# Kernel optimization log

Hardware: AMD Instinct MI355X
Metric: run time of the kernel (lower is better)

The kernel has to match this reference:

```python
import jax, jax.numpy as jnp
import numpy as np

TEMP = 0.07  # softmax temperature T


def _l2norm(x, axis=1, eps=1e-12):
    return x / jnp.clip(jnp.linalg.norm(x, axis=axis, keepdims=True), eps, None)


def setup_inputs() -> dict:
    key = jax.random.key(0)
    k1, k2, k3, k4 = jax.random.split(key, 4)
    B, K, D = 256, 8192, 128
    q = jax.random.normal(k1, (B, D), dtype=jnp.float32)
    ba_queue = _l2norm(jax.random.normal(k2, (K, D), dtype=jnp.float32))
    nonba_queue = _l2norm(jax.random.normal(k3, (K, D), dtype=jnp.float32))
    targets = jax.random.randint(k4, (B,), 0, 2, dtype=jnp.int64)
    return {"q": q, "ba_queue": ba_queue, "nonba_queue": nonba_queue, "targets": targets}


def reference(q, ba_queue, nonba_queue, targets):
    K = ba_queue.shape[0]
    # encoder output is L2-normalized; queues are detached buffers
    qn = _l2norm(q, axis=1)
    all_feature = jnp.concatenate([qn, ba_queue, nonba_queue], axis=0)  # [N, D]
    all_label = jnp.concatenate([
        targets.astype(jnp.int32),
        jnp.ones((K,), dtype=jnp.int32),
        jnp.zeros((K,), dtype=jnp.int32),
    ])  # [N]
    N = all_feature.shape[0]

    # [N, N] similarity logits
    sim = jnp.matmul(all_feature, all_feature.T) / TEMP
    logits = sim - jax.lax.stop_gradient(jnp.max(sim, axis=1, keepdims=True))

    # positive mask (same label), excluding self
    mask = (all_label[:, None] == all_label[None, :]).astype(jnp.float32)
    logits_mask = 1.0 - jnp.eye(N, dtype=jnp.float32)
    mask = mask * logits_mask

    exp_logits = jnp.exp(logits) * logits_mask
    log_prob = logits - jnp.log(jnp.sum(exp_logits, axis=1, keepdims=True))
    mean_log_prob_pos = jnp.sum(mask * log_prob, axis=1) / jnp.sum(mask, axis=1)
    return -jnp.mean(mean_log_prob_pos)
```

## Files before the change

### kernel.cpp

```cpp
#include <hip/hip_runtime.h>
#include <hip/hip_bf16.h>
#include <stdint.h>

#define TEMPERATURE 0.07f
#define SC 20.6099312f

constexpr int NQ = 256;
constexpr int KQ = 8192;
constexpr int D  = 128;
constexpr int N  = NQ + 2 * KQ;
constexpr int CS = 26;
constexpr int BN = 128;
constexpr int NT = N / BN;
constexpr int RBM = N / 128;
constexpr int RBF = N / 256;

typedef float f32x16 __attribute__((ext_vector_type(16)));
typedef int   i32x4  __attribute__((ext_vector_type(4)));
typedef int   i32x8  __attribute__((ext_vector_type(8)));

constexpr size_t OFF_F32  = 0;
constexpr size_t OFF_8    = OFF_F32  + (size_t)N * D * 4;
constexpr size_t OFF_8S   = OFF_8    + (size_t)N * D;
constexpr size_t OFF_PART = OFF_8S   + (size_t)N * D;
constexpr size_t OFF_LP   = OFF_PART + (size_t)CS * N * 4;
constexpr size_t OFF_S    = OFF_LP   + (size_t)260 * 2 * 128 * 4;
constexpr size_t OFF_CNT  = OFF_S    + 2 * 128 * 4;
constexpr size_t OFF_BSUM = OFF_CNT  + 16;

__global__ __launch_bounds__(256) void k_prep(const float* __restrict__ q,
                                              const float* __restrict__ ba,
                                              const float* __restrict__ nb,
                                              const long long* __restrict__ tgt,
                                              float* __restrict__ ff,
                                              unsigned char* __restrict__ fb8,
                                              unsigned char* __restrict__ fb8s,
                                              float* __restrict__ lp) {
    __shared__ float red[4][2][128];
    int wid = threadIdx.x >> 6, lane = threadIdx.x & 63;
    int rbase = blockIdx.x * 64 + wid * 16;
    float s0x = 0.f, s0y = 0.f, s1x = 0.f, s1y = 0.f;
    for (int i = 0; i < 16; ++i) {
        int r = rbase + i;
        const float* src = (r < NQ) ? (q + (size_t)r * D)
                         : (r < NQ + KQ) ? (ba + (size_t)(r - NQ) * D)
                         : (nb + (size_t)(r - NQ - KQ) * D);
        float2 v = *(const float2*)(src + lane * 2);
        float a = v.x, b = v.y;
        int lab;
        if (r < NQ) {
            float ss = a * a + b * b;
            #pragma unroll
            for (int m = 1; m < 64; m <<= 1) ss += __shfl_xor(ss, m);
            float scale = 1.0f / fmaxf(sqrtf(ss), 1e-12f);
            a *= scale; b *= scale;
            lab = (int)tgt[r];
        } else {
            lab = (r < NQ + KQ) ? 1 : 0;
        }
        *(float2*)(ff + (size_t)r * D + lane * 2) = make_float2(a, b);
        int w8  = __builtin_amdgcn_cvt_pk_fp8_f32(a, b, 0, false);
        int w8s = __builtin_amdgcn_cvt_pk_fp8_f32(a * SC, b * SC, 0, false);
        *(unsigned short*)(fb8  + (size_t)r * D + lane * 2) = (unsigned short)w8;
        *(unsigned short*)(fb8s + (size_t)r * D + lane * 2) = (unsigned short)w8s;
        if (lab) { s1x += a; s1y += b; } else { s0x += a; s0y += b; }
    }
    red[wid][0][lane * 2]     = s0x;
    red[wid][0][lane * 2 + 1] = s0y;
    red[wid][1][lane * 2]     = s1x;
    red[wid][1][lane * 2 + 1] = s1y;
    __syncthreads();
    int lab2 = threadIdx.x >> 7, d = threadIdx.x & 127;
    float s = red[0][lab2][d] + red[1][lab2][d] + red[2][lab2][d] + red[3][lab2][d];
    lp[((size_t)blockIdx.x * 2 + lab2) * 128 + d] = s;
}

__global__ __launch_bounds__(256) void k_lsum_b(const float* __restrict__ lp,
                                                const long long* __restrict__ tgt,
                                                float* __restrict__ S,
                                                int* __restrict__ cnt) {
    int lab = threadIdx.x >> 7;
    int d   = threadIdx.x & 127;
    float s[4] = {0.f, 0.f, 0.f, 0.f};
    for (int b = 0; b < 260; b += 4) {
        #pragma unroll
        for (int j = 0; j < 4; ++j)
            s[j] += lp[((size_t)(b + j) * 2 + lab) * 128 + d];
    }
    S[lab * 128 + d] = (s[0] + s[1]) + (s[2] + s[3]);
    if (threadIdx.x < 64) {
        int c = 0;
        #pragma unroll
        for (int i = 0; i < 4; ++i) c += (int)tgt[threadIdx.x + 64 * i];
        #pragma unroll
        for (int m = 1; m < 64; m <<= 1) c += __shfl_xor(c, m);
        if (threadIdx.x == 0) { cnt[0] = (NQ - c) + KQ; cnt[1] = c + KQ; }
    }
}

__global__ __launch_bounds__(256, 4) void k_main(const unsigned char* __restrict__ fb8,
                                                 const unsigned char* __restrict__ fb8s,
                                                 float* __restrict__ part) {
    __shared__ __align__(16) unsigned char lds[2][BN * 128];
    const int bid = blockIdx.x;
    const int rb = bid / CS, cs = bid % CS;
    const int tid = threadIdx.x;
    const int lane = tid & 63;
    const int wid  = tid >> 6;
    const int l31 = lane & 31, lhi = lane >> 5;
    const int rw = rb * 128 + wid * 32;

    int soff[4];
    #pragma unroll
    for (int i = 0; i < 4; ++i) {
        int flat = i * 256 + tid;
        int line = flat >> 4, p = flat & 15;
        int pl = p ^ (line & 15);
        soff[i] = (2 * line + (pl >> 3)) * 128 + (pl & 7) * 16;
    }

    i32x8 rf[2];
    #pragma unroll
    for (int s = 0; s < 2; ++s)
        rf[s] = *(const i32x8*)(fb8s + (size_t)(rw + l31) * D + s * 64 + lhi * 32);

    float rsum = 0.f;

    {
        const unsigned char* base = fb8 + (size_t)cs * (BN * 128);
        #pragma unroll
        for (int i = 0; i < 4; ++i)
            __builtin_amdgcn_global_load_lds(
                (const __attribute__((address_space(1))) unsigned int*)(base + soff[i]),
                (__attribute__((address_space(3))) unsigned int*)(&lds[0][(i * 256 + tid) * 16]),
                16, 0, 0);
    }
    asm volatile("s_waitcnt vmcnt(0)" ::: "memory");
    __builtin_amdgcn_s_barrier();

    int cur = 0;
    for (int t = 0; t < 5; ++t) {
        int ct = cs + t * CS;

        if (t + 1 < 5) {
            const unsigned char* base = fb8 + ((size_t)ct + CS) * (BN * 128);
            #pragma unroll
            for (int i = 0; i < 4; ++i)
                __builtin_amdgcn_global_load_lds(
                    (const __attribute__((address_space(1))) unsigned int*)(base + soff[i]),
                    (__attribute__((address_space(3))) unsigned int*)(&lds[cur ^ 1][(i * 256 + tid) * 16]),
                    16, 0, 0);
        }

        f32x16 acc[4];
        #pragma unroll
        for (int i = 0; i < 4; ++i)
            #pragma unroll
            for (int e = 0; e < 16; ++e) acc[i][e] = -SC;

        __builtin_amdgcn_s_setprio(1);
        #pragma unroll
        for (int s = 0; s < 2; ++s) {
            #pragma unroll
            for (int cc = 0; cc < 4; ++cc) {
                int crow = cc * 32 + l31;
                int line = crow >> 1;
                int pb = ((crow & 1) << 3) + s * 4 + lhi * 2;
                const unsigned char* lb = &lds[cur][line * 256];
                i32x4 lo = *(const i32x4*)(lb + ((pb    ) ^ (line & 15)) * 16);
                i32x4 hi = *(const i32x4*)(lb + ((pb + 1) ^ (line & 15)) * 16);
                i32x8 a = {lo[0], lo[1], lo[2], lo[3], hi[0], hi[1], hi[2], hi[3]};
                acc[cc] = __builtin_amdgcn_mfma_scale_f32_32x32x64_f8f6f4(
                    a, rf[s], acc[cc], 0, 0, 0, 0x7f7f7f7f, 0, 0x7f7f7f7f);
            }
        }
        __builtin_amdgcn_s_setprio(0);

        #pragma unroll
        for (int cc = 0; cc < 4; ++cc) {
            float p = 0.f;
            #pragma unroll
            for (int g = 0; g < 16; ++g)
                p += __builtin_amdgcn_exp2f(acc[cc][g]);
            rsum += p;
        }

        asm volatile("s_waitcnt vmcnt(0)" ::: "memory");
        __builtin_amdgcn_s_barrier();
        cur ^= 1;
    }

    rsum += __shfl_xor(rsum, 32);
    if (lane < 32)
        part[(size_t)cs * N + rw + lane] = rsum;
}

__global__ __launch_bounds__(256) void k_rowfin(const float* __restrict__ part,
                                                const float* __restrict__ ff,
                                                const float* __restrict__ S,
                                                const int* __restrict__ cnt,
                                                const long long* __restrict__ tgt,
                                                float* __restrict__ bsum) {
    __shared__ float sS[256];
    __shared__ float red[256];
    sS[threadIdx.x] = S[threadIdx.x];
    __syncthreads();
    int r = blockIdx.x * 256 + threadIdx.x;
    float se = 0.f;
    #pragma unroll
    for (int c = 0; c < CS; ++c) se += part[(size_t)c * N + r];
    int lab = (r < NQ) ? (int)tgt[r] : ((r < NQ + KQ) ? 1 : 0);
    const float4* frow = (const float4*)(ff + (size_t)r * D);
    const float4* srow = (const float4*)(sS + lab * 128);
    float dS = 0.f, dd = 0.f;
    #pragma unroll
    for (int i = 0; i < 32; ++i) {
        float4 f = frow[i];
        float4 s = srow[i];
        dS += f.x * s.x + f.y * s.y + f.z * s.z + f.w * s.w;
        int wa  = __builtin_amdgcn_cvt_pk_fp8_f32(f.x, f.y, 0, false);
        int wb  = __builtin_amdgcn_cvt_pk_fp8_f32(f.z, f.w, 0, false);
        int wsa = __builtin_amdgcn_cvt_pk_fp8_f32(f.x * SC, f.y * SC, 0, false);
        int wsb = __builtin_amdgcn_cvt_pk_fp8_f32(f.z * SC, f.w * SC, 0, false);
        dd += __builtin_amdgcn_cvt_f32_fp8(wa, 0) * __builtin_amdgcn_cvt_f32_fp8(wsa, 0)
            + __builtin_amdgcn_cvt_f32_fp8(wa, 1) * __builtin_amdgcn_cvt_f32_fp8(wsa, 1)
            + __builtin_amdgcn_cvt_f32_fp8(wb, 0) * __builtin_amdgcn_cvt_f32_fp8(wsb, 0)
            + __builtin_amdgcn_cvt_f32_fp8(wb, 1) * __builtin_amdgcn_cvt_f32_fp8(wsb, 1);
    }
    se -= __builtin_amdgcn_exp2f(dd - SC);
    float lse = logf(se) + 1.0f / TEMPERATURE;
    float P = (float)(cnt[lab] - 1);
    float mlpp = (dS - 1.0f) / (TEMPERATURE * P) - lse;
    red[threadIdx.x] = mlpp;
    __syncthreads();
    for (int s2 = 128; s2 > 0; s2 >>= 1) {
        if (threadIdx.x < s2) red[threadIdx.x] += red[threadIdx.x + s2];
        __syncthreads();
    }
    if (threadIdx.x == 0) bsum[blockIdx.x] = red[0];
}

__global__ __launch_bounds__(64) void k_final(const float* __restrict__ bsum,
                                              float* __restrict__ out) {
    float s = bsum[threadIdx.x];
    if (threadIdx.x == 0) s += bsum[64];
    #pragma unroll
    for (int m = 1; m < 64; m <<= 1) s += __shfl_xor(s, m);
    if (threadIdx.x == 0) out[0] = -s / (float)N;
}

extern "C" void kernel_launch(void* const* d_in, const int* in_sizes, int n_in,
                              void* d_out, int out_size, void* d_ws, size_t ws_size,
                              hipStream_t stream) {
    const float* q       = (const float*)d_in[0];
    const float* ba      = (const float*)d_in[1];
    const float* nb      = (const float*)d_in[2];
    const long long* tgt = (const long long*)d_in[3];
    char* ws = (char*)d_ws;
    float*         ff   = (float*)(ws + OFF_F32);
    unsigned char* fb8  = (unsigned char*)(ws + OFF_8);
    unsigned char* fb8s = (unsigned char*)(ws + OFF_8S);
    float*         part = (float*)(ws + OFF_PART);
    float*         lp   = (float*)(ws + OFF_LP);
    float*         S    = (float*)(ws + OFF_S);
    int*           cnt  = (int*)(ws + OFF_CNT);
    float*         bsum = (float*)(ws + OFF_BSUM);

    k_prep  <<<260,      256, 0, stream>>>(q, ba, nb, tgt, ff, fb8, fb8s, lp);
    k_lsum_b<<<1,        256, 0, stream>>>(lp, tgt, S, cnt);
    k_main  <<<RBM * CS, 256, 0, stream>>>(fb8, fb8s, part);
    k_rowfin<<<RBF,      256, 0, stream>>>(part, ff, S, cnt, tgt, bsum);
    k_final <<<1,         64, 0, stream>>>(bsum, (float*)d_out);
}
```

Before: 80.21 us.

## Use 2x2 warp tiling in main kernel and fold label-sum kernel into rowfin

The main kernel now arranges its four waves as a 2x2 grid. Each wave covers 64 rows by 64 columns, so every LDS tile load feeds two MFMAs, at the cost of more accumulators and register pressure (launch bounds lowered from 4 to 3). Each wave gets a partial row sum, and the two column halves are combined through shared memory. The separate single-block label-sum kernel is removed: each rowfin block recomputes the class sums and counts itself. This saves one launch but repeats that reduction in every block.

```diff
diff --git a/kernel.cpp b/kernel.cpp
--- a/kernel.cpp
+++ b/kernel.cpp
@@ -24,9 +24,7 @@
 constexpr size_t OFF_8S   = OFF_8    + (size_t)N * D;
 constexpr size_t OFF_PART = OFF_8S   + (size_t)N * D;
 constexpr size_t OFF_LP   = OFF_PART + (size_t)CS * N * 4;
-constexpr size_t OFF_S    = OFF_LP   + (size_t)260 * 2 * 128 * 4;
-constexpr size_t OFF_CNT  = OFF_S    + 2 * 128 * 4;
-constexpr size_t OFF_BSUM = OFF_CNT  + 16;
+constexpr size_t OFF_BSUM = OFF_LP   + (size_t)260 * 2 * 128 * 4;
 
 __global__ __launch_bounds__(256) void k_prep(const float* __restrict__ q,
                                               const float* __restrict__ ba,
@@ -75,30 +73,7 @@
     lp[((size_t)blockIdx.x * 2 + lab2) * 128 + d] = s;
 }
 
-__global__ __launch_bounds__(256) void k_lsum_b(const float* __restrict__ lp,
-                                                const long long* __restrict__ tgt,
-                                                float* __restrict__ S,
-                                                int* __restrict__ cnt) {
-    int lab = threadIdx.x >> 7;
-    int d   = threadIdx.x & 127;
-    float s[4] = {0.f, 0.f, 0.f, 0.f};
-    for (int b = 0; b < 260; b += 4) {
-        #pragma unroll
-        for (int j = 0; j < 4; ++j)
-            s[j] += lp[((size_t)(b + j) * 2 + lab) * 128 + d];
-    }
-    S[lab * 128 + d] = (s[0] + s[1]) + (s[2] + s[3]);
-    if (threadIdx.x < 64) {
-        int c = 0;
-        #pragma unroll
-        for (int i = 0; i < 4; ++i) c += (int)tgt[threadIdx.x + 64 * i];
-        #pragma unroll
-        for (int m = 1; m < 64; m <<= 1) c += __shfl_xor(c, m);
-        if (threadIdx.x == 0) { cnt[0] = (NQ - c) + KQ; cnt[1] = c + KQ; }
-    }
-}
-
-__global__ __launch_bounds__(256, 4) void k_main(const unsigned char* __restrict__ fb8,
+__global__ __launch_bounds__(256, 3) void k_main(const unsigned char* __restrict__ fb8,
                                                  const unsigned char* __restrict__ fb8s,
                                                  float* __restrict__ part) {
     __shared__ __align__(16) unsigned char lds[2][BN * 128];
@@ -107,8 +82,9 @@
     const int tid = threadIdx.x;
     const int lane = tid & 63;
     const int wid  = tid >> 6;
+    const int wr = wid >> 1, wc = wid & 1;
     const int l31 = lane & 31, lhi = lane >> 5;
-    const int rw = rb * 128 + wid * 32;
+    const int rw = rb * 128 + wr * 64;
 
     int soff[4];
     #pragma unroll
@@ -119,12 +95,14 @@
         soff[i] = (2 * line + (pl >> 3)) * 128 + (pl & 7) * 16;
     }
 
-    i32x8 rf[2];
-    #pragma unroll
-    for (int s = 0; s < 2; ++s)
-        rf[s] = *(const i32x8*)(fb8s + (size_t)(rw + l31) * D + s * 64 + lhi * 32);
-
-    float rsum = 0.f;
+    i32x8 rf[2][2];
+    #pragma unroll
+    for (int rs = 0; rs < 2; ++rs)
+        #pragma unroll
+        for (int s = 0; s < 2; ++s)
+            rf[rs][s] = *(const i32x8*)(fb8s + (size_t)(rw + rs * 32 + l31) * D + s * 64 + lhi * 32);
+
+    float rsum[2] = {0.f, 0.f};
 
     {
         const unsigned char* base = fb8 + (size_t)cs * (BN * 128);
@@ -152,37 +130,44 @@
                     16, 0, 0);
         }
 
-        f32x16 acc[4];
-        #pragma unroll
-        for (int i = 0; i < 4; ++i)
-            #pragma unroll
-            for (int e = 0; e < 16; ++e) acc[i][e] = -SC;
+        f32x16 acc[2][2];
+        #pragma unroll
+        for (int i = 0; i < 2; ++i)
+            #pragma unroll
+            for (int j = 0; j < 2; ++j)
+                #pragma unroll
+                for (int e = 0; e < 16; ++e) acc[i][j][e] = -SC;
 
         __builtin_amdgcn_s_setprio(1);
         #pragma unroll
         for (int s = 0; s < 2; ++s) {
             #pragma unroll
-            for (int cc = 0; cc < 4; ++cc) {
-                int crow = cc * 32 + l31;
+            for (int cc = 0; cc < 2; ++cc) {
+                int crow = wc * 64 + cc * 32 + l31;
                 int line = crow >> 1;
                 int pb = ((crow & 1) << 3) + s * 4 + lhi * 2;
                 const unsigned char* lb = &lds[cur][line * 256];
                 i32x4 lo = *(const i32x4*)(lb + ((pb    ) ^ (line & 15)) * 16);
                 i32x4 hi = *(const i32x4*)(lb + ((pb + 1) ^ (line & 15)) * 16);
                 i32x8 a = {lo[0], lo[1], lo[2], lo[3], hi[0], hi[1], hi[2], hi[3]};
-                acc[cc] = __builtin_amdgcn_mfma_scale_f32_32x32x64_f8f6f4(
-                    a, rf[s], acc[cc], 0, 0, 0, 0x7f7f7f7f, 0, 0x7f7f7f7f);
+                acc[cc][0] = __builtin_amdgcn_mfma_scale_f32_32x32x64_f8f6f4(
+                    a, rf[0][s], acc[cc][0], 0, 0, 0, 0x7f7f7f7f, 0, 0x7f7f7f7f);
+                acc[cc][1] = __builtin_amdgcn_mfma_scale_f32_32x32x64_f8f6f4(
+                    a, rf[1][s], acc[cc][1], 0, 0, 0, 0x7f7f7f7f, 0, 0x7f7f7f7f);
             }
         }
         __builtin_amdgcn_s_setprio(0);
 
         #pragma unroll
-        for (int cc = 0; cc < 4; ++cc) {
-            float p = 0.f;
-            #pragma unroll
-            for (int g = 0; g < 16; ++g)
-                p += __builtin_amdgcn_exp2f(acc[cc][g]);
-            rsum += p;
+        for (int cc = 0; cc < 2; ++cc) {
+            #pragma unroll
+            for (int rs = 0; rs < 2; ++rs) {
+                float p = 0.f;
+                #pragma unroll
+                for (int g = 0; g < 16; ++g)
+                    p += __builtin_amdgcn_exp2f(acc[cc][rs][g]);
+                rsum[rs] += p;
+            }
         }
 
         asm volatile("s_waitcnt vmcnt(0)" ::: "memory");
@@ -190,20 +175,46 @@
         cur ^= 1;
     }
 
-    rsum += __shfl_xor(rsum, 32);
-    if (lane < 32)
-        part[(size_t)cs * N + rw + lane] = rsum;
+    rsum[0] += __shfl_xor(rsum[0], 32);
+    rsum[1] += __shfl_xor(rsum[1], 32);
+    __shared__ float xred[2][2][32];
+    if (wc == 0 && lane < 32) {
+        xred[wr][0][lane] = rsum[0];
+        xred[wr][1][lane] = rsum[1];
+    }
+    __syncthreads();
+    if (wc == 1 && lane < 32) {
+        part[(size_t)cs * N + rw + lane]      = xred[wr][0][lane] + rsum[0];
+        part[(size_t)cs * N + rw + 32 + lane] = xred[wr][1][lane] + rsum[1];
+    }
 }
 
 __global__ __launch_bounds__(256) void k_rowfin(const float* __restrict__ part,
                                                 const float* __restrict__ ff,
-                                                const float* __restrict__ S,
-                                                const int* __restrict__ cnt,
+                                                const float* __restrict__ lp,
                                                 const long long* __restrict__ tgt,
                                                 float* __restrict__ bsum) {
     __shared__ float sS[256];
     __shared__ float red[256];
-    sS[threadIdx.x] = S[threadIdx.x];
+    __shared__ int scnt[2];
+    {
+        int lab = threadIdx.x >> 7, d = threadIdx.x & 127;
+        float s[4] = {0.f, 0.f, 0.f, 0.f};
+        for (int b = 0; b < 260; b += 4) {
+            #pragma unroll
+            for (int j = 0; j < 4; ++j)
+                s[j] += lp[((size_t)(b + j) * 2 + lab) * 128 + d];
+        }
+        sS[threadIdx.x] = (s[0] + s[1]) + (s[2] + s[3]);
+        if (threadIdx.x < 64) {
+            int c = 0;
+            #pragma unroll
+            for (int i = 0; i < 4; ++i) c += (int)tgt[threadIdx.x + 64 * i];
+            #pragma unroll
+            for (int m = 1; m < 64; m <<= 1) c += __shfl_xor(c, m);
+            if (threadIdx.x == 0) { scnt[0] = (NQ - c) + KQ; scnt[1] = c + KQ; }
+        }
+    }
     __syncthreads();
     int r = blockIdx.x * 256 + threadIdx.x;
     float se = 0.f;
@@ -229,7 +240,7 @@
     }
     se -= __builtin_amdgcn_exp2f(dd - SC);
     float lse = logf(se) + 1.0f / TEMPERATURE;
-    float P = (float)(cnt[lab] - 1);
+    float P = (float)(scnt[lab] - 1);
     float mlpp = (dS - 1.0f) / (TEMPERATURE * P) - lse;
     red[threadIdx.x] = mlpp;
     __syncthreads();
@@ -262,13 +273,10 @@
     unsigned char* fb8s = (unsigned char*)(ws + OFF_8S);
     float*         part = (float*)(ws + OFF_PART);
     float*         lp   = (float*)(ws + OFF_LP);
-    float*         S    = (float*)(ws + OFF_S);
-    int*           cnt  = (int*)(ws + OFF_CNT);
     float*         bsum = (float*)(ws + OFF_BSUM);
 
     k_prep  <<<260,      256, 0, stream>>>(q, ba, nb, tgt, ff, fb8, fb8s, lp);
-    k_lsum_b<<<1,        256, 0, stream>>>(lp, tgt, S, cnt);
     k_main  <<<RBM * CS, 256, 0, stream>>>(fb8, fb8s, part);
-    k_rowfin<<<RBF,      256, 0, stream>>>(part, ff, S, cnt, tgt, bsum);
+    k_rowfin<<<RBF,      256, 0, stream>>>(part, ff, lp, tgt, bsum);
     k_final <<<1,         64, 0, stream>>>(bsum, (float*)d_out);
 }
```

After: 77.95 us. 1.03x faster.
